# Performance work log

Hardware: AMD Instinct MI355X
Metric: run time of the kernel (lower is better)

## Reference

```python
import jax, jax.numpy as jnp
import numpy as np

TEMPERATURE = 0.05
K = 5
EPS = 1e-8
B, D = 4096, 512


def setup_inputs() -> dict:
    key = jax.random.key(0)
    k1, k2 = jax.random.split(key)
    f1 = jax.random.normal(k1, (B, D), dtype=jnp.float32)
    f2 = jax.random.normal(k2, (B, D), dtype=jnp.float32)
    # contrastive embeddings are typically L2-normalized; also keeps exp(dot/T) finite in fp32
    f1 = f1 / jnp.linalg.norm(f1, axis=-1, keepdims=True)
    f2 = f2 / jnp.linalg.norm(f2, axis=-1, keepdims=True)
    return {"features_1": f1, "features_2": f2}


def reference(features_1, features_2):
    b = features_1.shape[0]
    n = 2 * b
    feats = jnp.concatenate([features_1, features_2], axis=0)  # [2B, D]
    # cosine similarity via normalize + single GEMM (avoids O(N^2*D) broadcast)
    norms = jnp.linalg.norm(feats, axis=-1, keepdims=True)
    fn = feats / jnp.maximum(norms, EPS)
    sim = fn @ fn.T  # [2B, 2B]
    # k+1 nearest (self is the top-1 on the diagonal), drop first column
    _, nbr_idx = jax.lax.top_k(sim, K + 1)
    nbr_idx = nbr_idx[:, 1:]  # [2B, K]
    # positive pair term uses raw dot product (not cosine), as in the source
    pos = jnp.exp(jnp.sum(features_1 * features_2, axis=-1) / TEMPERATURE)  # [B]
    pos = jnp.concatenate([pos, pos], axis=0)  # [2B]
    neg = jnp.exp(sim / TEMPERATURE)  # [2B, 2B]
    diag = jnp.arange(n)
    neg = neg.at[diag, diag].set(0.0)  # mask self-similarity
    rows = diag[:, None]  # [2B, 1]
    neg = neg.at[rows, nbr_idx].set(0.0)  # zero out k nearest neighbors
    ng = jnp.sum(neg, axis=-1)  # [2B]
    loss = jnp.mean(-jnp.log(pos / (ng + pos)))
    return loss
```

## Files before the change

kernel.cpp:

```cpp
#include <hip/hip_runtime.h>
#include <hip/hip_bf16.h>

#define B_ROWS 4096
#define D_DIM  512
#define N_ROWS 8192
#define INV_T  20.0f
#define L2E_T  28.853900817779268f
#define EPS_N  1e-8f
#define CSPLIT 8
#define BM 256
#define BN 256
#define COLS_PER_CHUNK (N_ROWS / CSPLIT)
#define STRIPS (COLS_PER_CHUNK / BN)
#define NIT (STRIPS * 4)
#define HALF_BYTES 32768
#define BUF_BYTES  65536
#define PANEL_BYTES 131072
#define KITER_BYTES 32768

typedef __attribute__((ext_vector_type(16))) float floatx16;
typedef __attribute__((ext_vector_type(8)))  int   intx8;

#define AS1C(p) ((const __attribute__((address_space(1))) void*)(p))
#define AS3(p)  ((__attribute__((address_space(3))) void*)(p))

#define SC1 0x7F7F7F7F
#define MXMFMA(A, B, C) \
  __builtin_amdgcn_mfma_scale_f32_32x32x64_f8f6f4((A), (B), (C), 0, 0, 0, SC1, 0, SC1)

__device__ __forceinline__ intx8 ldsFrag32(const char* base, int row, int kgroup) {
  return *(const intx8*)(base + kgroup * 8192 + row * 32);
}

__device__ __forceinline__ void insert5(float (&t)[5], float v) {
  float n0 = fmaxf(t[0], v);
  float n1 = __builtin_amdgcn_fmed3f(v, t[1], t[0]);
  float n2 = __builtin_amdgcn_fmed3f(v, t[2], t[1]);
  float n3 = __builtin_amdgcn_fmed3f(v, t[3], t[2]);
  float n4 = __builtin_amdgcn_fmed3f(v, t[4], t[3]);
  t[0] = n0; t[1] = n1; t[2] = n2; t[3] = n3; t[4] = n4;
}

__device__ __forceinline__ void scan_acc(floatx16 (&acc)[2][2], float (&sum)[2],
                                         float (&top)[2][5]) {
  #pragma unroll
  for (int rb = 0; rb < 2; ++rb)
    #pragma unroll
    for (int cb = 0; cb < 2; ++cb)
      #pragma unroll
      for (int r = 0; r < 16; ++r) {
        float ev = exp2f(acc[rb][cb][r] * L2E_T);
        sum[rb] += ev;
        insert5(top[rb], ev);
      }
}

__device__ __forceinline__ void stage_tile(const char* gA_t, const char* gB_t,
                                           char* buf, int wave, int lane) {
  const char* src = ((wave < 8) ? gA_t : gB_t) + (wave & 7) * 4096 + lane * 16;
  char* dst = buf + ((wave < 8) ? 0 : HALF_BYTES) + (wave & 7) * 4096;
  #pragma unroll
  for (int q = 0; q < 4; ++q)
    __builtin_amdgcn_global_load_lds(AS1C(src + q * 1024), AS3(dst + q * 1024), 16, 0, 0);
}

__global__ __launch_bounds__(256) void prep_kernel(
    const float* __restrict__ f1, const float* __restrict__ f2,
    unsigned char* __restrict__ fnb8, float* __restrict__ dots)
{
  int row = blockIdx.x;
  int t = threadIdx.x;
  const float* r1 = f1 + (size_t)row * D_DIM;
  const float* r2 = f2 + (size_t)row * D_DIM;
  float2 a = *(const float2*)(r1 + 2 * t);
  float2 b = *(const float2*)(r2 + 2 * t);
  float s1 = a.x * a.x + a.y * a.y;
  float s2 = b.x * b.x + b.y * b.y;
  float d  = a.x * b.x + a.y * b.y;
  #pragma unroll
  for (int off = 32; off >= 1; off >>= 1) {
    s1 += __shfl_down(s1, off);
    s2 += __shfl_down(s2, off);
    d  += __shfl_down(d, off);
  }
  __shared__ float red[4][3];
  __shared__ float bc[2];
  int wave = t >> 6, lane = t & 63;
  if (lane == 0) { red[wave][0] = s1; red[wave][1] = s2; red[wave][2] = d; }
  __syncthreads();
  if (t == 0) {
    float S1 = red[0][0] + red[1][0] + red[2][0] + red[3][0];
    float S2 = red[0][1] + red[1][1] + red[2][1] + red[3][1];
    float Dd = red[0][2] + red[1][2] + red[2][2] + red[3][2];
    bc[0] = 1.0f / fmaxf(sqrtf(S1), EPS_N);
    bc[1] = 1.0f / fmaxf(sqrtf(S2), EPS_N);
    dots[row] = Dd;
  }
  __syncthreads();
  if (t < 128) {
    int q = t & 63;
    int is2 = t >> 6;
    const float* src = (is2 ? f2 : f1) + (size_t)row * D_DIM + q * 8;
    float sc = bc[is2];
    float4 v0 = *(const float4*)(src);
    float4 v1 = *(const float4*)(src + 4);
    int lo = __builtin_amdgcn_cvt_pk_fp8_f32(v0.x * sc, v0.y * sc, 0, false);
    lo     = __builtin_amdgcn_cvt_pk_fp8_f32(v0.z * sc, v0.w * sc, lo, true);
    int hi = __builtin_amdgcn_cvt_pk_fp8_f32(v1.x * sc, v1.y * sc, 0, false);
    hi     = __builtin_amdgcn_cvt_pk_fp8_f32(v1.z * sc, v1.w * sc, hi, true);
    int grow = row + is2 * B_ROWS;
    int panel = grow >> 8, rin = grow & 255;
    int kgroup = q >> 2, inner = (q & 3) * 8;
    int2 pack; pack.x = lo; pack.y = hi;
    *(int2*)(fnb8 + (size_t)panel * PANEL_BYTES + kgroup * 8192 + rin * 32 + inner) = pack;
  }
}

__global__ __launch_bounds__(1024, 4) void sim_kernel(
    const unsigned char* __restrict__ fnb8,
    float* __restrict__ partials)
{
  __shared__ int4 lds4[8192];
  char* lds = (char*)lds4;

  int bx = blockIdx.x;
  int xcd = bx & 7, kk = bx >> 3;
  int rt = xcd * 4 + (kk & 3);
  int chunk = kk >> 2;
  int rowbase = rt * BM;
  int chunkbase = chunk * COLS_PER_CHUNK;

  int t = threadIdx.x;
  int wave = t >> 6, lane = t & 63;
  int wr = wave >> 2, wc = wave & 3;
  int l31 = lane & 31, lh = lane >> 5;

  float sum[2];
  float top[2][5];
  floatx16 acc[2][2];
  #pragma unroll
  for (int rb = 0; rb < 2; ++rb) {
    sum[rb] = 0.f;
    #pragma unroll
    for (int k = 0; k < 5; ++k) top[rb][k] = 0.f;
    #pragma unroll
    for (int cb = 0; cb < 2; ++cb)
      #pragma unroll
      for (int e = 0; e < 16; ++e) acc[rb][cb][e] = 0.0f;
  }

  const char* gA  = (const char*)fnb8 + (size_t)rt * PANEL_BYTES;
  const char* gB0 = (const char*)fnb8 + (size_t)(chunk * 4) * PANEL_BYTES;

  stage_tile(gA, gB0, lds, wave, lane);
  __syncthreads();

  for (int it = 0; it < NIT; ++it) {
    int strip = it >> 2, kstep = it & 3, cur = it & 1;

    if (it + 1 < NIT) {
      int ns = (it + 1) >> 2, nk = (it + 1) & 3;
      stage_tile(gA + nk * KITER_BYTES,
                 gB0 + (size_t)ns * PANEL_BYTES + nk * KITER_BYTES,
                 lds + (cur ^ 1) * BUF_BYTES, wave, lane);
    }

    const char* As = lds + cur * BUF_BYTES;
    const char* Bs = As + HALF_BYTES;
    __builtin_amdgcn_s_setprio(1);
    #pragma unroll
    for (int m = 0; m < 2; ++m) {
      int kg = m * 2 + lh;
      intx8 rf0 = ldsFrag32(As, wr * 64 + l31,      kg);
      intx8 rf1 = ldsFrag32(As, wr * 64 + 32 + l31, kg);
      intx8 cf0 = ldsFrag32(Bs, wc * 64 + l31,      kg);
      intx8 cf1 = ldsFrag32(Bs, wc * 64 + 32 + l31, kg);
      acc[0][0] = MXMFMA(cf0, rf0, acc[0][0]);
      acc[0][1] = MXMFMA(cf1, rf0, acc[0][1]);
      acc[1][0] = MXMFMA(cf0, rf1, acc[1][0]);
      acc[1][1] = MXMFMA(cf1, rf1, acc[1][1]);
    }
    __builtin_amdgcn_s_setprio(0);

    if (kstep == 3) {
      bool dwave = (rowbase + wr * 64) == (chunkbase + strip * BN + wc * 64);
      if (dwave && (((l31 >> 2) & 1) == lh)) {
        int rd = (l31 & 3) | (((l31 >> 3) & 3) << 2);
        acc[0][0][rd] = -1e30f;
        acc[1][1][rd] = -1e30f;
      }
      scan_acc(acc, sum, top);
      #pragma unroll
      for (int rb = 0; rb < 2; ++rb)
        #pragma unroll
        for (int cb = 0; cb < 2; ++cb)
          #pragma unroll
          for (int e = 0; e < 16; ++e) acc[rb][cb][e] = 0.0f;
    }

    __syncthreads();
  }

  #pragma unroll
  for (int rb = 0; rb < 2; ++rb) {
    sum[rb] += __shfl_xor(sum[rb], 32);
    float pt[5];
    #pragma unroll
    for (int k = 0; k < 5; ++k) pt[k] = __shfl_xor(top[rb][k], 32);
    #pragma unroll
    for (int k = 0; k < 5; ++k) insert5(top[rb], pt[k]);
  }

  float* mbuf = (float*)lds;
  if (lane < 32) {
    #pragma unroll
    for (int rb = 0; rb < 2; ++rb) {
      float* dst = mbuf + (size_t)(((wave * 2 + rb) * 32) + lane) * 6;
      dst[0] = sum[rb];
      #pragma unroll
      for (int k = 0; k < 5; ++k) dst[1 + k] = top[rb][k];
    }
  }
  __syncthreads();
  if (t < 256) {
    int wr2 = t >> 6, rb2 = (t >> 5) & 1, r31 = t & 31;
    float s = 0.0f;
    float a5[5] = {0.f, 0.f, 0.f, 0.f, 0.f};
    #pragma unroll
    for (int wc2 = 0; wc2 < 4; ++wc2) {
      int w = wr2 * 4 + wc2;
      const float* src = mbuf + (size_t)(((w * 2 + rb2) * 32) + r31) * 6;
      s += src[0];
      #pragma unroll
      for (int k = 0; k < 5; ++k) insert5(a5, src[1 + k]);
    }
    int grow = rowbase + t;
    float* dst = partials + ((size_t)grow * CSPLIT + chunk) * 6;
    dst[0] = s;
    #pragma unroll
    for (int k = 0; k < 5; ++k) dst[1 + k] = a5[k];
  }
}

__global__ __launch_bounds__(256) void finalize1_kernel(
    const float* __restrict__ partials, const float* __restrict__ dots,
    float* __restrict__ bpart)
{
  int row = blockIdx.x * 256 + threadIdx.x;
  const float* p = partials + (size_t)row * (CSPLIT * 6);
  float s = 0.0f;
  float a5[5] = {0.f, 0.f, 0.f, 0.f, 0.f};
  #pragma unroll
  for (int c = 0; c < CSPLIT; ++c) {
    s += p[c * 6];
    #pragma unroll
    for (int k = 0; k < 5; ++k) insert5(a5, p[c * 6 + 1 + k]);
  }
  float ng = s - (a5[0] + a5[1] + a5[2] + a5[3] + a5[4]);
  float dv = dots[row & (B_ROWS - 1)];
  float acc = __logf(ng + __expf(dv * INV_T)) - dv * INV_T;

  #pragma unroll
  for (int off = 32; off >= 1; off >>= 1) acc += __shfl_down(acc, off);
  __shared__ float red[4];
  int wave = threadIdx.x >> 6, lane = threadIdx.x & 63;
  if (lane == 0) red[wave] = acc;
  __syncthreads();
  if (threadIdx.x == 0)
    bpart[blockIdx.x] = red[0] + red[1] + red[2] + red[3];
}

__global__ __launch_bounds__(64) void finalize2_kernel(
    const float* __restrict__ bpart, float* __restrict__ out)
{
  int t = threadIdx.x;
  float v = (t < 32) ? bpart[t] : 0.0f;
  #pragma unroll
  for (int off = 32; off >= 1; off >>= 1) v += __shfl_down(v, off);
  if (t == 0) out[0] = v / (float)N_ROWS;
}

extern "C" void kernel_launch(void* const* d_in, const int* in_sizes, int n_in,
                              void* d_out, int out_size, void* d_ws, size_t ws_size,
                              hipStream_t stream) {
  const float* f1 = (const float*)d_in[0];
  const float* f2 = (const float*)d_in[1];
  float* out = (float*)d_out;
  char* ws = (char*)d_ws;

  unsigned char* fnb8 = (unsigned char*)ws;
  float* dots = (float*)(ws + (size_t)4 * 1024 * 1024);
  float* partials = (float*)(ws + (size_t)4 * 1024 * 1024 + 65536);
  float* bpart = (float*)(ws + (size_t)8 * 1024 * 1024);

  prep_kernel<<<B_ROWS, 256, 0, stream>>>(f1, f2, fnb8, dots);
  sim_kernel<<<(N_ROWS / BM) * CSPLIT, 1024, 0, stream>>>(fnb8, partials);
  finalize1_kernel<<<32, 256, 0, stream>>>(partials, dots, bpart);
  finalize2_kernel<<<1, 64, 0, stream>>>(bpart, out);
}
```

Baseline: 67.22 us.

## Shrink column tile to 128 and read row fragments directly from global

The column strip width is halved so each wave computes a 64x32 block with two accumulators instead of four. Only the B tile is staged through LDS (16 KB per buffer, down from 64 KB), while the A row-panel fragments are loaded straight from global memory each k-iteration. The prep kernel now writes fp8 data in a split-half layout that matches these 16-byte loads. The aim is to cut LDS use and staging traffic and raise occupancy, at the cost of repeated global or cache reads of A and fewer MFMAs per synchronisation.

```diff
diff --git a/kernel.cpp b/kernel.cpp
--- a/kernel.cpp
+++ b/kernel.cpp
@@ -9,28 +9,24 @@
 #define EPS_N  1e-8f
 #define CSPLIT 8
 #define BM 256
-#define BN 256
+#define BN 128
 #define COLS_PER_CHUNK (N_ROWS / CSPLIT)
 #define STRIPS (COLS_PER_CHUNK / BN)
 #define NIT (STRIPS * 4)
-#define HALF_BYTES 32768
-#define BUF_BYTES  65536
+#define BUF_BYTES 16384
 #define PANEL_BYTES 131072
-#define KITER_BYTES 32768
 
 typedef __attribute__((ext_vector_type(16))) float floatx16;
 typedef __attribute__((ext_vector_type(8)))  int   intx8;
+typedef __attribute__((ext_vector_type(4)))  int   intx4;
 
 #define AS1C(p) ((const __attribute__((address_space(1))) void*)(p))
 #define AS3(p)  ((__attribute__((address_space(3))) void*)(p))
+#define CAT8(a, b) __builtin_shufflevector((a), (b), 0, 1, 2, 3, 4, 5, 6, 7)
 
 #define SC1 0x7F7F7F7F
 #define MXMFMA(A, B, C) \
   __builtin_amdgcn_mfma_scale_f32_32x32x64_f8f6f4((A), (B), (C), 0, 0, 0, SC1, 0, SC1)
-
-__device__ __forceinline__ intx8 ldsFrag32(const char* base, int row, int kgroup) {
-  return *(const intx8*)(base + kgroup * 8192 + row * 32);
-}
 
 __device__ __forceinline__ void insert5(float (&t)[5], float v) {
   float n0 = fmaxf(t[0], v);
@@ -41,27 +37,16 @@
   t[0] = n0; t[1] = n1; t[2] = n2; t[3] = n3; t[4] = n4;
 }
 
-__device__ __forceinline__ void scan_acc(floatx16 (&acc)[2][2], float (&sum)[2],
+__device__ __forceinline__ void scan_acc(floatx16 (&acc)[2], float (&sum)[2],
                                          float (&top)[2][5]) {
   #pragma unroll
   for (int rb = 0; rb < 2; ++rb)
     #pragma unroll
-    for (int cb = 0; cb < 2; ++cb)
-      #pragma unroll
-      for (int r = 0; r < 16; ++r) {
-        float ev = exp2f(acc[rb][cb][r] * L2E_T);
-        sum[rb] += ev;
-        insert5(top[rb], ev);
-      }
-}
-
-__device__ __forceinline__ void stage_tile(const char* gA_t, const char* gB_t,
-                                           char* buf, int wave, int lane) {
-  const char* src = ((wave < 8) ? gA_t : gB_t) + (wave & 7) * 4096 + lane * 16;
-  char* dst = buf + ((wave < 8) ? 0 : HALF_BYTES) + (wave & 7) * 4096;
-  #pragma unroll
-  for (int q = 0; q < 4; ++q)
-    __builtin_amdgcn_global_load_lds(AS1C(src + q * 1024), AS3(dst + q * 1024), 16, 0, 0);
+    for (int r = 0; r < 16; ++r) {
+      float ev = exp2f(acc[rb][r] * L2E_T);
+      sum[rb] += ev;
+      insert5(top[rb], ev);
+    }
 }
 
 __global__ __launch_bounds__(256) void prep_kernel(
@@ -110,9 +95,12 @@
     hi     = __builtin_amdgcn_cvt_pk_fp8_f32(v1.z * sc, v1.w * sc, hi, true);
     int grow = row + is2 * B_ROWS;
     int panel = grow >> 8, rin = grow & 255;
-    int kgroup = q >> 2, inner = (q & 3) * 8;
+    int kg = q >> 2;
+    int rem = q & 3;
+    int half = rem >> 1, inner = (rem & 1) * 8;
     int2 pack; pack.x = lo; pack.y = hi;
-    *(int2*)(fnb8 + (size_t)panel * PANEL_BYTES + kgroup * 8192 + rin * 32 + inner) = pack;
+    *(int2*)(fnb8 + (size_t)panel * PANEL_BYTES + kg * 8192 + half * 4096
+             + rin * 16 + inner) = pack;
   }
 }
 
@@ -120,7 +108,7 @@
     const unsigned char* __restrict__ fnb8,
     float* __restrict__ partials)
 {
-  __shared__ int4 lds4[8192];
+  __shared__ int4 lds4[2048];
   char* lds = (char*)lds4;
 
   int bx = blockIdx.x;
@@ -135,67 +123,73 @@
   int wr = wave >> 2, wc = wave & 3;
   int l31 = lane & 31, lh = lane >> 5;
 
+  int r0 = wr * 64 + l31;
+  int r1 = r0 + 32;
+  int bcol16 = (wc * 32 + l31) * 16;
+
+  int skg = wave >> 2, shalf = (wave >> 1) & 1, ssub = wave & 1;
+  int soff = skg * 4096 + shalf * 2048 + ssub * 1024 + lane * 16;
+  int sgsub = shalf * 4096 + ssub * 1024 + lane * 16;
+
   float sum[2];
   float top[2][5];
-  floatx16 acc[2][2];
+  floatx16 acc[2];
   #pragma unroll
   for (int rb = 0; rb < 2; ++rb) {
     sum[rb] = 0.f;
     #pragma unroll
     for (int k = 0; k < 5; ++k) top[rb][k] = 0.f;
     #pragma unroll
-    for (int cb = 0; cb < 2; ++cb)
-      #pragma unroll
-      for (int e = 0; e < 16; ++e) acc[rb][cb][e] = 0.0f;
+    for (int e = 0; e < 16; ++e) acc[rb][e] = 0.0f;
   }
 
   const char* gA  = (const char*)fnb8 + (size_t)rt * PANEL_BYTES;
   const char* gB0 = (const char*)fnb8 + (size_t)(chunk * 4) * PANEL_BYTES;
 
-  stage_tile(gA, gB0, lds, wave, lane);
+  __builtin_amdgcn_global_load_lds(AS1C(gB0 + skg * 8192 + sgsub),
+                                   AS3(lds + soff), 16, 0, 0);
   __syncthreads();
 
   for (int it = 0; it < NIT; ++it) {
-    int strip = it >> 2, kstep = it & 3, cur = it & 1;
+    int strip = it >> 2, kiter = it & 3, cur = it & 1;
 
     if (it + 1 < NIT) {
       int ns = (it + 1) >> 2, nk = (it + 1) & 3;
-      stage_tile(gA + nk * KITER_BYTES,
-                 gB0 + (size_t)ns * PANEL_BYTES + nk * KITER_BYTES,
-                 lds + (cur ^ 1) * BUF_BYTES, wave, lane);
-    }
-
-    const char* As = lds + cur * BUF_BYTES;
-    const char* Bs = As + HALF_BYTES;
+      const char* bp = gB0 + (size_t)(ns >> 1) * PANEL_BYTES + ((ns & 1) * 128) * 16;
+      __builtin_amdgcn_global_load_lds(AS1C(bp + (nk * 4 + skg) * 8192 + sgsub),
+                                       AS3(lds + (cur ^ 1) * BUF_BYTES + soff), 16, 0, 0);
+    }
+
+    const char* Bs = lds + cur * BUF_BYTES;
     __builtin_amdgcn_s_setprio(1);
     #pragma unroll
     for (int m = 0; m < 2; ++m) {
       int kg = m * 2 + lh;
-      intx8 rf0 = ldsFrag32(As, wr * 64 + l31,      kg);
-      intx8 rf1 = ldsFrag32(As, wr * 64 + 32 + l31, kg);
-      intx8 cf0 = ldsFrag32(Bs, wc * 64 + l31,      kg);
-      intx8 cf1 = ldsFrag32(Bs, wc * 64 + 32 + l31, kg);
-      acc[0][0] = MXMFMA(cf0, rf0, acc[0][0]);
-      acc[0][1] = MXMFMA(cf1, rf0, acc[0][1]);
-      acc[1][0] = MXMFMA(cf0, rf1, acc[1][0]);
-      acc[1][1] = MXMFMA(cf1, rf1, acc[1][1]);
+      const char* abase = gA + (kiter * 4 + kg) * 8192;
+      intx4 a00 = *(const intx4*)(abase + r0 * 16);
+      intx4 a01 = *(const intx4*)(abase + 4096 + r0 * 16);
+      intx4 a10 = *(const intx4*)(abase + r1 * 16);
+      intx4 a11 = *(const intx4*)(abase + 4096 + r1 * 16);
+      const char* bbase = Bs + kg * 4096 + bcol16;
+      intx4 b0 = *(const intx4*)(bbase);
+      intx4 b1 = *(const intx4*)(bbase + 2048);
+      intx8 cf = CAT8(b0, b1);
+      acc[0] = MXMFMA(cf, CAT8(a00, a01), acc[0]);
+      acc[1] = MXMFMA(cf, CAT8(a10, a11), acc[1]);
     }
     __builtin_amdgcn_s_setprio(0);
 
-    if (kstep == 3) {
-      bool dwave = (rowbase + wr * 64) == (chunkbase + strip * BN + wc * 64);
-      if (dwave && (((l31 >> 2) & 1) == lh)) {
+    if (kiter == 3) {
+      int d = (chunkbase + strip * BN + wc * 32) - (rowbase + wr * 64);
+      if ((d == 0 || d == 32) && lh == ((l31 >> 2) & 1)) {
         int rd = (l31 & 3) | (((l31 >> 3) & 3) << 2);
-        acc[0][0][rd] = -1e30f;
-        acc[1][1][rd] = -1e30f;
+        acc[d >> 5][rd] = -1e30f;
       }
       scan_acc(acc, sum, top);
       #pragma unroll
       for (int rb = 0; rb < 2; ++rb)
         #pragma unroll
-        for (int cb = 0; cb < 2; ++cb)
-          #pragma unroll
-          for (int e = 0; e < 16; ++e) acc[rb][cb][e] = 0.0f;
+        for (int e = 0; e < 16; ++e) acc[rb][e] = 0.0f;
     }
 
     __syncthreads();
@@ -212,6 +206,7 @@
   }
 
   float* mbuf = (float*)lds;
+  __syncthreads();
   if (lane < 32) {
     #pragma unroll
     for (int rb = 0; rb < 2; ++rb) {
```

Measured after the change: 106.3 us. 1.58x slower.

## Quantize normalized features to FP4 and use FP4 scaled MFMA for similarity GEMM

Applied to the files above, without the earlier changes.

Normalized features are encoded as FP4 (E2M1) with a scale of 32 instead of FP8. The similarity GEMM uses the f8f6f4 MFMA in FP4 mode, and the exp factor is rescaled to undo the 32x32 scaling. This halves the global and LDS bytes per tile and uses the higher-rate FP4 matrix path, but FP4 precision is very coarse. That risks wrong top-k neighbor selection and loss values outside tolerance.

```diff
diff --git a/kernel.cpp b/kernel.cpp
--- a/kernel.cpp
+++ b/kernel.cpp
@@ -4,32 +4,33 @@
 #define B_ROWS 4096
 #define D_DIM  512
 #define N_ROWS 8192
+#define EPS_N  1e-8f
 #define INV_T  20.0f
-#define L2E_T  28.853900817779268f
-#define EPS_N  1e-8f
+#define FACT   0.0281778328298626f
 #define CSPLIT 8
 #define BM 256
 #define BN 256
 #define COLS_PER_CHUNK (N_ROWS / CSPLIT)
 #define STRIPS (COLS_PER_CHUNK / BN)
 #define NIT (STRIPS * 4)
-#define HALF_BYTES 32768
-#define BUF_BYTES  65536
-#define PANEL_BYTES 131072
-#define KITER_BYTES 32768
+#define TILE_BYTES 16384
+#define BUF_BYTES  32768
+#define PANEL_BYTES 65536
+#define KITER_BYTES 16384
 
 typedef __attribute__((ext_vector_type(16))) float floatx16;
 typedef __attribute__((ext_vector_type(8)))  int   intx8;
+typedef __attribute__((ext_vector_type(4)))  int   intx4;
 
 #define AS1C(p) ((const __attribute__((address_space(1))) void*)(p))
 #define AS3(p)  ((__attribute__((address_space(3))) void*)(p))
 
 #define SC1 0x7F7F7F7F
-#define MXMFMA(A, B, C) \
-  __builtin_amdgcn_mfma_scale_f32_32x32x64_f8f6f4((A), (B), (C), 0, 0, 0, SC1, 0, SC1)
-
-__device__ __forceinline__ intx8 ldsFrag32(const char* base, int row, int kgroup) {
-  return *(const intx8*)(base + kgroup * 8192 + row * 32);
+#define MXMFMA4(A, B, C) \
+  __builtin_amdgcn_mfma_scale_f32_32x32x64_f8f6f4((A), (B), (C), 4, 4, 0, SC1, 0, SC1)
+
+__device__ __forceinline__ intx4 ldsFrag16(const char* base, int row, int kg) {
+  return *(const intx4*)(base + kg * 4096 + row * 16);
 }
 
 __device__ __forceinline__ void insert5(float (&t)[5], float v) {
@@ -49,24 +50,33 @@
     for (int cb = 0; cb < 2; ++cb)
       #pragma unroll
       for (int r = 0; r < 16; ++r) {
-        float ev = exp2f(acc[rb][cb][r] * L2E_T);
+        float ev = exp2f(acc[rb][cb][r] * FACT);
         sum[rb] += ev;
         insert5(top[rb], ev);
       }
 }
 
+__device__ __forceinline__ unsigned enc_fp4(float y) {
+  float f = fminf(fabsf(y), 6.0f);
+  float c1 = rintf(f + f);
+  float c2 = rintf(f - 2.0f) + 4.0f;
+  float c3 = rintf((f - 4.0f) * 0.5f) + 6.0f;
+  float c = (f < 2.0f) ? c1 : ((f < 4.0f) ? c2 : c3);
+  return (unsigned)c | ((__float_as_uint(y) >> 31) << 3);
+}
+
 __device__ __forceinline__ void stage_tile(const char* gA_t, const char* gB_t,
                                            char* buf, int wave, int lane) {
-  const char* src = ((wave < 8) ? gA_t : gB_t) + (wave & 7) * 4096 + lane * 16;
-  char* dst = buf + ((wave < 8) ? 0 : HALF_BYTES) + (wave & 7) * 4096;
-  #pragma unroll
-  for (int q = 0; q < 4; ++q)
+  const char* src = ((wave < 8) ? gA_t : gB_t) + (wave & 7) * 2048 + lane * 16;
+  char* dst = buf + ((wave < 8) ? 0 : TILE_BYTES) + (wave & 7) * 2048;
+  #pragma unroll
+  for (int q = 0; q < 2; ++q)
     __builtin_amdgcn_global_load_lds(AS1C(src + q * 1024), AS3(dst + q * 1024), 16, 0, 0);
 }
 
 __global__ __launch_bounds__(256) void prep_kernel(
     const float* __restrict__ f1, const float* __restrict__ f2,
-    unsigned char* __restrict__ fnb8, float* __restrict__ dots)
+    unsigned char* __restrict__ fnb4, float* __restrict__ dots)
 {
   int row = blockIdx.x;
   int t = threadIdx.x;
@@ -101,26 +111,30 @@
     int q = t & 63;
     int is2 = t >> 6;
     const float* src = (is2 ? f2 : f1) + (size_t)row * D_DIM + q * 8;
-    float sc = bc[is2];
+    float sc = bc[is2] * 32.0f;
     float4 v0 = *(const float4*)(src);
     float4 v1 = *(const float4*)(src + 4);
-    int lo = __builtin_amdgcn_cvt_pk_fp8_f32(v0.x * sc, v0.y * sc, 0, false);
-    lo     = __builtin_amdgcn_cvt_pk_fp8_f32(v0.z * sc, v0.w * sc, lo, true);
-    int hi = __builtin_amdgcn_cvt_pk_fp8_f32(v1.x * sc, v1.y * sc, 0, false);
-    hi     = __builtin_amdgcn_cvt_pk_fp8_f32(v1.z * sc, v1.w * sc, hi, true);
+    unsigned p = enc_fp4(v0.x * sc);
+    p |= enc_fp4(v0.y * sc) << 4;
+    p |= enc_fp4(v0.z * sc) << 8;
+    p |= enc_fp4(v0.w * sc) << 12;
+    p |= enc_fp4(v1.x * sc) << 16;
+    p |= enc_fp4(v1.y * sc) << 20;
+    p |= enc_fp4(v1.z * sc) << 24;
+    p |= enc_fp4(v1.w * sc) << 28;
     int grow = row + is2 * B_ROWS;
     int panel = grow >> 8, rin = grow & 255;
-    int kgroup = q >> 2, inner = (q & 3) * 8;
-    int2 pack; pack.x = lo; pack.y = hi;
-    *(int2*)(fnb8 + (size_t)panel * PANEL_BYTES + kgroup * 8192 + rin * 32 + inner) = pack;
+    int kg = q >> 2;
+    *(unsigned*)(fnb4 + (size_t)panel * PANEL_BYTES + kg * 4096 + rin * 16
+                 + (q & 3) * 4) = p;
   }
 }
 
 __global__ __launch_bounds__(1024, 4) void sim_kernel(
-    const unsigned char* __restrict__ fnb8,
+    const unsigned char* __restrict__ fnb4,
     float* __restrict__ partials)
 {
-  __shared__ int4 lds4[8192];
+  __shared__ int4 lds4[4096];
   char* lds = (char*)lds4;
 
   int bx = blockIdx.x;
@@ -149,12 +163,13 @@
       for (int e = 0; e < 16; ++e) acc[rb][cb][e] = 0.0f;
   }
 
-  const char* gA  = (const char*)fnb8 + (size_t)rt * PANEL_BYTES;
-  const char* gB0 = (const char*)fnb8 + (size_t)(chunk * 4) * PANEL_BYTES;
+  const char* gA  = (const char*)fnb4 + (size_t)rt * PANEL_BYTES;
+  const char* gB0 = (const char*)fnb4 + (size_t)(chunk * 4) * PANEL_BYTES;
 
   stage_tile(gA, gB0, lds, wave, lane);
   __syncthreads();
 
+  intx4 z4 = {0, 0, 0, 0};
   for (int it = 0; it < NIT; ++it) {
     int strip = it >> 2, kstep = it & 3, cur = it & 1;
 
@@ -166,19 +181,23 @@
     }
 
     const char* As = lds + cur * BUF_BYTES;
-    const char* Bs = As + HALF_BYTES;
+    const char* Bs = As + TILE_BYTES;
     __builtin_amdgcn_s_setprio(1);
     #pragma unroll
     for (int m = 0; m < 2; ++m) {
       int kg = m * 2 + lh;
-      intx8 rf0 = ldsFrag32(As, wr * 64 + l31,      kg);
-      intx8 rf1 = ldsFrag32(As, wr * 64 + 32 + l31, kg);
-      intx8 cf0 = ldsFrag32(Bs, wc * 64 + l31,      kg);
-      intx8 cf1 = ldsFrag32(Bs, wc * 64 + 32 + l31, kg);
-      acc[0][0] = MXMFMA(cf0, rf0, acc[0][0]);
-      acc[0][1] = MXMFMA(cf1, rf0, acc[0][1]);
-      acc[1][0] = MXMFMA(cf0, rf1, acc[1][0]);
-      acc[1][1] = MXMFMA(cf1, rf1, acc[1][1]);
+      intx4 rf0 = ldsFrag16(As, wr * 64 + l31,      kg);
+      intx4 rf1 = ldsFrag16(As, wr * 64 + 32 + l31, kg);
+      intx4 cf0 = ldsFrag16(Bs, wc * 64 + l31,      kg);
+      intx4 cf1 = ldsFrag16(Bs, wc * 64 + 32 + l31, kg);
+      intx8 R0 = __builtin_shufflevector(rf0, z4, 0, 1, 2, 3, 4, 5, 6, 7);
+      intx8 R1 = __builtin_shufflevector(rf1, z4, 0, 1, 2, 3, 4, 5, 6, 7);
+      intx8 C0 = __builtin_shufflevector(cf0, z4, 0, 1, 2, 3, 4, 5, 6, 7);
+      intx8 C1 = __builtin_shufflevector(cf1, z4, 0, 1, 2, 3, 4, 5, 6, 7);
+      acc[0][0] = MXMFMA4(C0, R0, acc[0][0]);
+      acc[0][1] = MXMFMA4(C1, R0, acc[0][1]);
+      acc[1][0] = MXMFMA4(C0, R1, acc[1][0]);
+      acc[1][1] = MXMFMA4(C1, R1, acc[1][1]);
     }
     __builtin_amdgcn_s_setprio(0);
 
@@ -288,13 +307,13 @@
   float* out = (float*)d_out;
   char* ws = (char*)d_ws;
 
-  unsigned char* fnb8 = (unsigned char*)ws;
+  unsigned char* fnb4 = (unsigned char*)ws;
   float* dots = (float*)(ws + (size_t)4 * 1024 * 1024);
   float* partials = (float*)(ws + (size_t)4 * 1024 * 1024 + 65536);
   float* bpart = (float*)(ws + (size_t)8 * 1024 * 1024);
 
-  prep_kernel<<<B_ROWS, 256, 0, stream>>>(f1, f2, fnb8, dots);
-  sim_kernel<<<(N_ROWS / BM) * CSPLIT, 1024, 0, stream>>>(fnb8, partials);
+  prep_kernel<<<B_ROWS, 256, 0, stream>>>(f1, f2, fnb4, dots);
+  sim_kernel<<<(N_ROWS / BM) * CSPLIT, 1024, 0, stream>>>(fnb4, partials);
   finalize1_kernel<<<32, 256, 0, stream>>>(partials, dots, bpart);
   finalize2_kernel<<<1, 64, 0, stream>>>(bpart, out);
 }
```

Measured after the change: 59.80 us. -11.0%, faster.
